# Optimization experiments

Hardware: AMD Instinct MI355X
Metric: run time of the kernel (lower is better)

Reference implementation:

```python
import jax, jax.numpy as jnp
import numpy as np

CH = 64
CF = CH // 8  # f/g projection channels


def setup_inputs() -> dict:
    key = jax.random.key(0)
    k1, k2, k3, k4, k5 = jax.random.split(key, 5)
    x = jax.random.normal(k1, (8, 64, 64, CH), dtype=jnp.float32)
    kernel_f = 0.02 * jax.random.normal(k2, (1, 1, CH, CF), dtype=jnp.float32)
    kernel_g = 0.02 * jax.random.normal(k3, (1, 1, CH, CF), dtype=jnp.float32)
    kernel_h = 0.02 * jax.random.normal(k4, (1, 1, CH, CH), dtype=jnp.float32)
    gamma = 0.02 * jax.random.normal(k5, (1,), dtype=jnp.float32)
    return {"x": x, "kernel_f": kernel_f, "kernel_g": kernel_g,
            "kernel_h": kernel_h, "gamma": gamma}


def reference(x, kernel_f, kernel_g, kernel_h, gamma):
    B, H, W, C = x.shape
    N = H * W
    xf = x.reshape(B, N, C)  # flatten spatial; 1x1 conv == matmul over channels
    f = jnp.einsum('bnc,cd->bnd', xf, kernel_f[0, 0])  # [B,N,CF]
    g = jnp.einsum('bnc,cd->bnd', xf, kernel_g[0, 0])  # [B,N,CF]
    h = jnp.einsum('bnc,cd->bnd', xf, kernel_h[0, 0])  # [B,N,C]
    s = jnp.einsum('bnd,bmd->bnm', g, f)  # g @ f^T, [B,N,N]
    beta = jax.nn.softmax(s, axis=-1)
    o = jnp.einsum('bnm,bmc->bnc', beta, h)  # [B,N,C]
    out = gamma * o.reshape(B, H, W, C) + x
    return out
```

## Files before the change

kernel.cpp:

```cpp
#include <hip/hip_runtime.h>
#include <hip/hip_bf16.h>

typedef __attribute__((ext_vector_type(4)))  float f32x4;
typedef __attribute__((ext_vector_type(16))) float f32x16;
typedef __attribute__((ext_vector_type(8)))  short bf16x8;

#define LOG2E 1.44269504088896340736f

#if __has_builtin(__builtin_amdgcn_exp2f)
static __device__ __forceinline__ float exp2_native(float x) {
  return __builtin_amdgcn_exp2f(x);
}
#else
extern "C" __device__ float __ocml_native_exp2_f32(float);
static __device__ __forceinline__ float exp2_native(float x) {
  return __ocml_native_exp2_f32(x);
}
#endif

static __device__ __forceinline__ unsigned int pack_trunc_f(float a, float b) {
  return __builtin_amdgcn_perm(__float_as_uint(b), __float_as_uint(a), 0x07060302);
}

typedef const __attribute__((address_space(1))) unsigned int gu32;
typedef __attribute__((address_space(3))) unsigned int lu32;
static __device__ __forceinline__ void gload_lds16(const void* g, void* l) {
  __builtin_amdgcn_global_load_lds((gu32*)g, (lu32*)l, 16, 0, 0);
}

__global__ __launch_bounds__(256) void proj_kernel(
    const float* __restrict__ x, const float* __restrict__ kf,
    const float* __restrict__ kg, const float* __restrict__ kh,
    unsigned short* __restrict__ f_b, unsigned short* __restrict__ g_b,
    unsigned short* __restrict__ h_p)
{
  __shared__ unsigned short Kt[80*72];
  const int t = threadIdx.x, blk = blockIdx.x;

  #pragma unroll
  for (int r = 0; r < 20; ++r) {
    int idx = r*256 + t;
    int o = idx >> 6, c = idx & 63;
    float v = (o < 8) ? kf[c*8 + o]
            : (o < 16) ? kg[c*8 + (o-8)] * LOG2E
            : kh[c*64 + (o-16)];
    Kt[o*72 + c] = (unsigned short)(__float_as_uint(v) >> 16);
  }
  __syncthreads();

  const int w = t >> 6, lane = t & 63, l15 = lane & 15, quad = lane >> 4;
  const int Rbase = blk*64 + w*16;
  const int R = Rbase + l15;

  bf16x8 af[2];
  #pragma unroll
  for (int kk = 0; kk < 2; ++kk) {
    const float* xp = x + (long)R*64 + kk*32 + quad*8;
    float4 v0 = *(const float4*)xp;
    float4 v1 = *(const float4*)(xp + 4);
    union { unsigned int u[4]; bf16x8 v; } p;
    p.u[0] = pack_trunc_f(v0.x, v0.y);
    p.u[1] = pack_trunc_f(v0.z, v0.w);
    p.u[2] = pack_trunc_f(v1.x, v1.y);
    p.u[3] = pack_trunc_f(v1.z, v1.w);
    af[kk] = p.v;
  }

  f32x4 acc[5];
  #pragma unroll
  for (int nt = 0; nt < 5; ++nt) { f32x4 z = {}; acc[nt] = z; }

  #pragma unroll
  for (int nt = 0; nt < 5; ++nt)
    #pragma unroll
    for (int kk = 0; kk < 2; ++kk) {
      bf16x8 bfv = *(const bf16x8*)&Kt[(nt*16 + l15)*72 + kk*32 + quad*8];
      acc[nt] = __builtin_amdgcn_mfma_f32_16x16x32_bf16(af[kk], bfv, acc[nt], 0, 0, 0);
    }

  const int bt = Rbase >> 12;
  const int kt = (Rbase >> 7) & 31;
  const int base = ((blk & 1) << 6) + (w << 4);
  const int pi = base + ((quad & 1) << 3) + (((quad >> 1) & 1) << 2);

  #pragma unroll
  for (int rr = 0; rr < 4; ++rr) {
    const int nq = (Rbase + quad*4 + rr) & 4095;
    unsigned short v = (unsigned short)(__float_as_uint(acc[0][rr]) >> 16);
    if (l15 < 8) f_b[((long)bt*4096 + nq)*8 + l15] = v;
    else         g_b[((long)bt*4096 + nq)*8 + (l15 - 8)] = v;
  }
  #pragma unroll
  for (int nt = 1; nt < 5; ++nt) {
    const int c = (nt - 1)*16 + l15;
    uint2 v;
    v.x = pack_trunc_f(acc[nt][0], acc[nt][1]);
    v.y = pack_trunc_f(acc[nt][2], acc[nt][3]);
    *(uint2*)(h_p + ((long)(bt*32 + kt)*64 + c)*136 + pi) = v;
  }
}

__global__ __launch_bounds__(256, 2) void attn_kernel(
    const unsigned short* __restrict__ f_b, const unsigned short* __restrict__ g_b,
    const unsigned short* __restrict__ h_p,
    const float* __restrict__ x, const float* __restrict__ gamma_p,
    float* __restrict__ out)
{
  extern __shared__ char smem[];

  const int t = threadIdx.x;
  const int w = t >> 6, lane = t & 63, l31 = lane & 31, a = lane >> 5;
  const int qg = w & 1, kh = w >> 1;
  const int qb = blockIdx.x, b = blockIdx.y;
  const int q0w = qb*64 + qg*32;

  bf16x8 gfv;
  {
    bf16x8 gv = *(const bf16x8*)(g_b + ((long)b*4096 + q0w + l31)*8);
    bf16x8 z = {};
    gfv = (a == 0) ? gv : z;
  }
  bf16x8 bhl;
  {
    union { unsigned short s[8]; bf16x8 v; } o8;
    #pragma unroll
    for (int j = 0; j < 8; ++j) o8.s[j] = 0x3F80;
    bf16x8 z = {};
    bhl = (l31 == 0) ? o8.v : z;
  }

  f32x16 oacc[2], ol;
  { f32x16 z = {}; oacc[0] = z; oacc[1] = z; ol = z; }

  const char* hp_b = (const char*)h_p + (long)b*32*17408;
  const char* fb_b = (const char*)f_b + (long)b*4096*16;
  char* sbase = smem + kh*38912;

  auto stage = [&](int bi, int ktl) {
    const int kt = kh*16 + ktl;
    const char* hsrc = hp_b + (long)kt*17408;
    const char* fsrc = fb_b + (long)kt*2048;
    char* dst = sbase + bi*19456;
    #pragma unroll
    for (int i = 0; i < 10; ++i) {
      const int c = i*2 + qg;
      if (c < 19) {
        const int off = c*1024;
        const char* src = (off < 17408) ? (hsrc + off) : (fsrc + (off - 17408));
        gload_lds16(src + lane*16, dst + off);
      }
    }
  };

  stage(0, 0);

  for (int ktl = 0; ktl < 16; ++ktl) {
    __syncthreads();
    if (ktl < 15) stage((ktl + 1) & 1, ktl + 1);

    const unsigned short* hts = (const unsigned short*)(sbase + (ktl & 1)*19456);
    const unsigned short* fts = hts + 8704;

    #pragma unroll
    for (int mt = 0; mt < 4; ++mt) {
      bf16x8 afv = *(const bf16x8*)&fts[(mt*32 + l31)*8];
      f32x16 zz = {};
      f32x16 sc = __builtin_amdgcn_mfma_f32_32x32x16_bf16(afv, gfv, zz, 0, 0, 0);

      #pragma unroll
      for (int half = 0; half < 2; ++half) {
        const int s = mt*2 + half;
        bf16x8 bh0 = *(const bf16x8*)&hts[(l31)*136      + s*16 + a*8];
        bf16x8 bh1 = *(const bf16x8*)&hts[(32 + l31)*136 + s*16 + a*8];
        union { unsigned int u[4]; bf16x8 v; } ap;
        #pragma unroll
        for (int j = 0; j < 4; ++j) {
          float ea = exp2_native(sc[half*8 + 2*j]);
          float eb = exp2_native(sc[half*8 + 2*j + 1]);
          ap.u[j] = pack_trunc_f(ea, eb);
        }
        oacc[0] = __builtin_amdgcn_mfma_f32_32x32x16_bf16(ap.v, bh0, oacc[0], 0, 0, 0);
        oacc[1] = __builtin_amdgcn_mfma_f32_32x32x16_bf16(ap.v, bh1, oacc[1], 0, 0, 0);
        ol      = __builtin_amdgcn_mfma_f32_32x32x16_bf16(ap.v, bhl, ol,      0, 0, 0);
      }
    }
  }

  __syncthreads();
  float* cb = (float*)smem;
  if (kh == 1) {
    float* d = cb + (qg*64 + lane)*48;
    #pragma unroll
    for (int r = 0; r < 16; ++r) {
      d[r] = oacc[0][r]; d[16 + r] = oacc[1][r]; d[32 + r] = ol[r];
    }
  }
  __syncthreads();
  if (kh == 0) {
    const float* sp = cb + (qg*64 + lane)*48;
    #pragma unroll
    for (int r = 0; r < 16; ++r) {
      oacc[0][r] += sp[r]; oacc[1][r] += sp[16 + r]; ol[r] += sp[32 + r];
    }

    const float gamma = gamma_p[0];
    const float* xb = x + ((long)b*4096 + q0w)*64;
    float* ob = out + ((long)b*4096 + q0w)*64;

    #pragma unroll
    for (int r = 0; r < 16; ++r) {
      const int q = (r & 3) + 8*(r >> 2) + 4*a;
      const float lq = __shfl(ol[r], lane & 32);
      const float s = gamma / lq;
      #pragma unroll
      for (int nt = 0; nt < 2; ++nt) {
        const long idx = (long)q*64 + nt*32 + l31;
        ob[idx] = fmaf(s, oacc[nt][r], xb[idx]);
      }
    }
  }
}

extern "C" void kernel_launch(void* const* d_in, const int* in_sizes, int n_in,
                              void* d_out, int out_size, void* d_ws, size_t ws_size,
                              hipStream_t stream) {
  const float* x  = (const float*)d_in[0];
  const float* kf = (const float*)d_in[1];
  const float* kg = (const float*)d_in[2];
  const float* kh = (const float*)d_in[3];
  const float* gamma = (const float*)d_in[4];
  float* out = (float*)d_out;

  char* ws = (char*)d_ws;
  unsigned short* h_p = (unsigned short*)ws;
  unsigned short* f_b = (unsigned short*)(ws + 4456448);
  unsigned short* g_b = (unsigned short*)(ws + 4980736);

  proj_kernel<<<512, 256, 0, stream>>>(x, kf, kg, kh, f_b, g_b, h_p);
  attn_kernel<<<dim3(64, 8), 256, 77824, stream>>>(f_b, g_b, h_p, x, gamma, out);
}
```

Before: 109.3 us.

## Split attention key dimension across four waves with 32-query blocks

After: 111.3 us. Within noise of the previous version (+1.9%).

```diff
diff --git a/kernel.cpp b/kernel.cpp
--- a/kernel.cpp
+++ b/kernel.cpp
@@ -100,7 +100,7 @@
   }
 }
 
-__global__ __launch_bounds__(256, 2) void attn_kernel(
+__global__ __launch_bounds__(256, 4) void attn_kernel(
     const unsigned short* __restrict__ f_b, const unsigned short* __restrict__ g_b,
     const unsigned short* __restrict__ h_p,
     const float* __restrict__ x, const float* __restrict__ gamma_p,
@@ -110,13 +110,12 @@
 
   const int t = threadIdx.x;
   const int w = t >> 6, lane = t & 63, l31 = lane & 31, a = lane >> 5;
-  const int qg = w & 1, kh = w >> 1;
   const int qb = blockIdx.x, b = blockIdx.y;
-  const int q0w = qb*64 + qg*32;
+  const int q0 = qb*32;
 
   bf16x8 gfv;
   {
-    bf16x8 gv = *(const bf16x8*)(g_b + ((long)b*4096 + q0w + l31)*8);
+    bf16x8 gv = *(const bf16x8*)(g_b + ((long)b*4096 + q0 + l31)*8);
     bf16x8 z = {};
     gfv = (a == 0) ? gv : z;
   }
@@ -134,16 +133,14 @@
 
   const char* hp_b = (const char*)h_p + (long)b*32*17408;
   const char* fb_b = (const char*)f_b + (long)b*4096*16;
-  char* sbase = smem + kh*38912;
-
-  auto stage = [&](int bi, int ktl) {
-    const int kt = kh*16 + ktl;
+
+  auto stage = [&](int bi, int kt) {
     const char* hsrc = hp_b + (long)kt*17408;
     const char* fsrc = fb_b + (long)kt*2048;
-    char* dst = sbase + bi*19456;
-    #pragma unroll
-    for (int i = 0; i < 10; ++i) {
-      const int c = i*2 + qg;
+    char* dst = smem + bi*19456;
+    #pragma unroll
+    for (int i = 0; i < 5; ++i) {
+      const int c = i*4 + w;
       if (c < 19) {
         const int off = c*1024;
         const char* src = (off < 17408) ? (hsrc + off) : (fsrc + (off - 17408));
@@ -154,58 +151,58 @@
 
   stage(0, 0);
 
-  for (int ktl = 0; ktl < 16; ++ktl) {
+  for (int ktl = 0; ktl < 32; ++ktl) {
     __syncthreads();
-    if (ktl < 15) stage((ktl + 1) & 1, ktl + 1);
-
-    const unsigned short* hts = (const unsigned short*)(sbase + (ktl & 1)*19456);
+    if (ktl < 31) stage((ktl + 1) & 1, ktl + 1);
+
+    const unsigned short* hts = (const unsigned short*)(smem + (ktl & 1)*19456);
     const unsigned short* fts = hts + 8704;
 
-    #pragma unroll
-    for (int mt = 0; mt < 4; ++mt) {
-      bf16x8 afv = *(const bf16x8*)&fts[(mt*32 + l31)*8];
-      f32x16 zz = {};
-      f32x16 sc = __builtin_amdgcn_mfma_f32_32x32x16_bf16(afv, gfv, zz, 0, 0, 0);
-
+    bf16x8 afv = *(const bf16x8*)&fts[(w*32 + l31)*8];
+    f32x16 zz = {};
+    f32x16 sc = __builtin_amdgcn_mfma_f32_32x32x16_bf16(afv, gfv, zz, 0, 0, 0);
+
+    #pragma unroll
+    for (int half = 0; half < 2; ++half) {
+      const int s = w*2 + half;
+      bf16x8 bh0 = *(const bf16x8*)&hts[(l31)*136      + s*16 + a*8];
+      bf16x8 bh1 = *(const bf16x8*)&hts[(32 + l31)*136 + s*16 + a*8];
+      union { unsigned int u[4]; bf16x8 v; } ap;
       #pragma unroll
-      for (int half = 0; half < 2; ++half) {
-        const int s = mt*2 + half;
-        bf16x8 bh0 = *(const bf16x8*)&hts[(l31)*136      + s*16 + a*8];
-        bf16x8 bh1 = *(const bf16x8*)&hts[(32 + l31)*136 + s*16 + a*8];
-        union { unsigned int u[4]; bf16x8 v; } ap;
-        #pragma unroll
-        for (int j = 0; j < 4; ++j) {
-          float ea = exp2_native(sc[half*8 + 2*j]);
-          float eb = exp2_native(sc[half*8 + 2*j + 1]);
-          ap.u[j] = pack_trunc_f(ea, eb);
-        }
-        oacc[0] = __builtin_amdgcn_mfma_f32_32x32x16_bf16(ap.v, bh0, oacc[0], 0, 0, 0);
-        oacc[1] = __builtin_amdgcn_mfma_f32_32x32x16_bf16(ap.v, bh1, oacc[1], 0, 0, 0);
-        ol      = __builtin_amdgcn_mfma_f32_32x32x16_bf16(ap.v, bhl, ol,      0, 0, 0);
-      }
+      for (int j = 0; j < 4; ++j) {
+        float ea = exp2_native(sc[half*8 + 2*j]);
+        float eb = exp2_native(sc[half*8 + 2*j + 1]);
+        ap.u[j] = pack_trunc_f(ea, eb);
+      }
+      oacc[0] = __builtin_amdgcn_mfma_f32_32x32x16_bf16(ap.v, bh0, oacc[0], 0, 0, 0);
+      oacc[1] = __builtin_amdgcn_mfma_f32_32x32x16_bf16(ap.v, bh1, oacc[1], 0, 0, 0);
+      ol      = __builtin_amdgcn_mfma_f32_32x32x16_bf16(ap.v, bhl, ol,      0, 0, 0);
     }
   }
 
   __syncthreads();
   float* cb = (float*)smem;
-  if (kh == 1) {
-    float* d = cb + (qg*64 + lane)*48;
+  if (w > 0) {
+    float* d = cb + ((w - 1)*64 + lane)*49;
     #pragma unroll
     for (int r = 0; r < 16; ++r) {
       d[r] = oacc[0][r]; d[16 + r] = oacc[1][r]; d[32 + r] = ol[r];
     }
   }
   __syncthreads();
-  if (kh == 0) {
-    const float* sp = cb + (qg*64 + lane)*48;
-    #pragma unroll
-    for (int r = 0; r < 16; ++r) {
-      oacc[0][r] += sp[r]; oacc[1][r] += sp[16 + r]; ol[r] += sp[32 + r];
+  if (w == 0) {
+    #pragma unroll
+    for (int sl = 0; sl < 3; ++sl) {
+      const float* sp = cb + (sl*64 + lane)*49;
+      #pragma unroll
+      for (int r = 0; r < 16; ++r) {
+        oacc[0][r] += sp[r]; oacc[1][r] += sp[16 + r]; ol[r] += sp[32 + r];
+      }
     }
 
     const float gamma = gamma_p[0];
-    const float* xb = x + ((long)b*4096 + q0w)*64;
-    float* ob = out + ((long)b*4096 + q0w)*64;
+    const float* xb = x + ((long)b*4096 + q0)*64;
+    float* ob = out + ((long)b*4096 + q0)*64;
 
     #pragma unroll
     for (int r = 0; r < 16; ++r) {
@@ -237,5 +234,5 @@
   unsigned short* g_b = (unsigned short*)(ws + 4980736);
 
   proj_kernel<<<512, 256, 0, stream>>>(x, kf, kg, kh, f_b, g_b, h_p);
-  attn_kernel<<<dim3(64, 8), 256, 77824, stream>>>(f_b, g_b, h_p, x, gamma, out);
-}
+  attn_kernel<<<dim3(128, 8), 256, 38912, stream>>>(f_b, g_b, h_p, x, gamma, out);
+}
```
